# Kernel tuning notes

Measured on AMD Instinct MI355X. Metric: run time of the kernel, lower is better.

Reference implementation:

```python
import jax, jax.numpy as jnp
import numpy as np
from jax import lax

B, CHI, CHO, H, W = 8, 128, 128, 64, 64
K = 3
KK = K * K


def setup_inputs() -> dict:
    key = jax.random.key(0)
    ks = jax.random.split(key, 7)
    x = jax.random.normal(ks[0], (B, CHI, H, W), jnp.float32)
    # small offset-conv weights so sampled offsets stay in a realistic few-pixel range
    off_w = jax.random.normal(ks[1], (3 * KK, CHI, K, K), jnp.float32) * 0.01
    off_b = jnp.zeros((3 * KK,), jnp.float32)
    w = jax.random.normal(ks[2], (CHO, CHI, K, K), jnp.float32) / np.sqrt(CHI * KK).astype(np.float32)
    b = jnp.zeros((CHO,), jnp.float32)
    gamma = jax.random.uniform(ks[3], (CHO,), jnp.float32)  # nn.init.uniform_ on BN weight
    beta = jnp.zeros((CHO,), jnp.float32)
    return {"x": x, "off_w": off_w, "off_b": off_b, "w": w, "b": b, "gamma": gamma, "beta": beta}


def _deform_conv(x, off_w, off_b, w, b):
    """DCNv2 modulated deformable conv, k=3, stride=1, pad=1, dil=1, 1 deform group."""
    B_, C, H_, W_ = x.shape
    # offset/mask branch: plain 3x3 conv -> 27 channels (2*9 offsets, 9 masks)
    om = lax.conv_general_dilated(x, off_w, (1, 1), ((1, 1), (1, 1)),
                                  dimension_numbers=("NCHW", "OIHW", "NCHW"))
    om = om + off_b[None, :, None, None]
    off = om[:, : 2 * KK].reshape(B_, KK, 2, H_, W_)  # [B,9,2,H,W]; ch 2k=y, 2k+1=x
    mask = jax.nn.sigmoid(om[:, 2 * KK:])             # [B,9,H,W]

    ky, kx = jnp.meshgrid(jnp.arange(K, dtype=jnp.float32),
                          jnp.arange(K, dtype=jnp.float32), indexing="ij")
    ky = ky.reshape(KK); kx = kx.reshape(KK)
    # sampling positions: p = p0 - pad + k*dil + offset
    py = off[:, :, 0] + (jnp.arange(H_, dtype=jnp.float32) - 1.0)[None, None, :, None] + ky[None, :, None, None]
    px = off[:, :, 1] + (jnp.arange(W_, dtype=jnp.float32) - 1.0)[None, None, None, :] + kx[None, :, None, None]

    y0 = jnp.floor(py); x0 = jnp.floor(px)
    ly = py - y0; lx = px - x0
    xf = x.reshape(B_, C, H_ * W_)

    def corner(yi, xi, wgt):
        valid = ((yi >= 0) & (yi <= H_ - 1) & (xi >= 0) & (xi <= W_ - 1)).astype(x.dtype)
        yc = jnp.clip(yi, 0, H_ - 1).astype(jnp.int32)
        xc = jnp.clip(xi, 0, W_ - 1).astype(jnp.int32)
        idx = (yc * W_ + xc).reshape(B_, KK * H_ * W_)
        g = jax.vmap(lambda xb, ib: xb[:, ib])(xf, idx).reshape(B_, C, KK, H_, W_)
        return g * (valid * wgt)[:, None]

    val = (corner(y0, x0, (1 - ly) * (1 - lx))
           + corner(y0, x0 + 1, (1 - ly) * lx)
           + corner(y0 + 1, x0, ly * (1 - lx))
           + corner(y0 + 1, x0 + 1, ly * lx))  # [B,C,9,H,W]
    val = val * mask[:, None]  # modulation
    out = jnp.einsum("bckhw,ock->bohw", val, w.reshape(w.shape[0], C, KK))
    return out + b[None, :, None, None]


def reference(x, off_w, off_b, w, b, gamma, beta):
    y = _deform_conv(x, off_w, off_b, w, b)
    # BatchNorm2d in training mode (batch statistics), eps=1e-5, then ReLU
    mean = y.mean(axis=(0, 2, 3))
    var = y.var(axis=(0, 2, 3))
    yn = (y - mean[None, :, None, None]) * lax.rsqrt(var[None, :, None, None] + 1e-5)
    return jax.nn.relu(yn * gamma[None, :, None, None] + beta[None, :, None, None])
```

## Files before the change

kernel.cpp:

```cpp
#include <hip/hip_runtime.h>
#include <hip/hip_bf16.h>
#include <math.h>

#define HH 64
#define WW 64
#define HW 4096
#define LDV 136

typedef __bf16 bf16x8 __attribute__((ext_vector_type(8)));
typedef float floatx4 __attribute__((ext_vector_type(4)));
typedef unsigned int uint4a __attribute__((ext_vector_type(4)));
typedef unsigned int uint2a __attribute__((ext_vector_type(2)));

#define WS_Y    0u
#define WS_XTB  16777216u
#define WS_WTB  25165824u
#define WS_OWB  25460736u
#define WS_PSQ  25534464u

static __device__ inline ushort f2bf(float f) {
  __hip_bfloat16 h = __float2bfloat16(f);
  return __builtin_bit_cast(ushort, h);
}
static __device__ inline float lo16(unsigned int u) { return __builtin_bit_cast(float, u << 16); }
static __device__ inline float hi16(unsigned int u) { return __builtin_bit_cast(float, u & 0xffff0000u); }

static __device__ inline void barrier_lds() {
  asm volatile("s_waitcnt lgkmcnt(0)" ::: "memory");
  __builtin_amdgcn_s_barrier();
}

__global__ __launch_bounds__(256) void k_prep(const float* __restrict__ x,
                                              const float* __restrict__ w,
                                              const float* __restrict__ ow,
                                              ushort* __restrict__ xtb,
                                              ushort* __restrict__ wtb,
                                              ushort* __restrict__ owb,
                                              float* __restrict__ psq) {
  __shared__ float tile[32][33];
  int bid = blockIdx.x;
  if (bid < 4096) {
    int hw0 = (bid & 127) * 32;
    int c0 = ((bid >> 7) & 3) * 32;
    int b = bid >> 9;
    int col = threadIdx.x & 31, row = threadIdx.x >> 5;
    const float* xb = x + ((size_t)b * 128 + c0) * HW + hw0;
#pragma unroll
    for (int i = 0; i < 32; i += 8)
      tile[row + i][col] = xb[(size_t)(row + i) * HW + col];
    __syncthreads();
    int hw = threadIdx.x >> 3, cq = threadIdx.x & 7;
    ushort* xo = xtb + ((size_t)b * HW + hw0) * 128 + c0;
    unsigned int lo = (unsigned int)f2bf(tile[cq * 4 + 0][hw]) |
                      ((unsigned int)f2bf(tile[cq * 4 + 1][hw]) << 16);
    unsigned int hi = (unsigned int)f2bf(tile[cq * 4 + 2][hw]) |
                      ((unsigned int)f2bf(tile[cq * 4 + 3][hw]) << 16);
    uint2a v2 = (uint2a){lo, hi};
    *(uint2a*)(&xo[(size_t)hw * 128 + cq * 4]) = v2;
  } else if (bid < 4096 + 576) {
    int idx = (bid - 4096) * 256 + threadIdx.x;
    int c = idx & 127, o = (idx >> 7) & 127, k = idx >> 14;
    wtb[idx] = f2bf(w[(o * 128 + c) * 9 + k]);
  } else if (bid < 4096 + 720) {
    int j = (bid - 4672) * 256 + threadIdx.x;
    int c = j & 127, o = (j >> 7) & 31, k = j >> 12;
    float v = (o < 27) ? ow[(o * 128 + c) * 9 + k] : 0.f;
    owb[j] = f2bf(v);
  } else {
    for (int i = threadIdx.x; i < 2048; i += 256) psq[i] = 0.f;
  }
}

__global__ __launch_bounds__(256) void k_main(
    const ushort* __restrict__ xtb, const ushort* __restrict__ wtb,
    const ushort* __restrict__ owb, const float* __restrict__ off_b,
    const float* __restrict__ bias, float* __restrict__ y,
    float* __restrict__ psq) {
  __shared__ ushort Vl[2][16 * LDV];
  __shared__ float omL[27 * 16];
  int t = threadIdx.x;
  int lane = t & 63, wv = t >> 6;
  int li = lane & 15, quad = lane >> 4;
  int bx = blockIdx.x;
  int row = bx >> 2, p0b = (bx & 3) * 16;
  int b = blockIdx.y;
  const ushort* xb = xtb + (size_t)b * HW * 128;
  int ch = t & 15;
  int pq = t >> 4;

  int mi = wv;
  floatx4 oacc = (floatx4){0.f, 0.f, 0.f, 0.f};
  uint4a u0;
  auto p1load = [&](int k, uint4a& u) {
    int ky = k / 3, kx = k % 3;
    int ry = row - 1 + ky, cx = p0b + pq - 1 + kx;
    bool v = (ry >= 0 && ry < HH && cx >= 0 && cx < WW);
    int idx = v ? (ry * WW + cx) : 0;
    uint4a a = *(const uint4a*)(xb + (size_t)idx * 128 + ch * 8);
    u = v ? a : (uint4a){0u, 0u, 0u, 0u};
  };
  p1load(0, u0);
  for (int k = 0; k < 9; ++k) {
    *(uint4a*)(&Vl[k & 1][pq * LDV + ch * 8]) = u0;
    if (k < 8) p1load(k + 1, u0);
    barrier_lds();
    if (wv < 2) {
#pragma unroll
      for (int ks = 0; ks < 4; ++ks) {
        bf16x8 bfrag = __builtin_bit_cast(bf16x8,
            *(const uint4a*)(&Vl[k & 1][li * LDV + ks * 32 + quad * 8]));
        bf16x8 afrag = __builtin_bit_cast(bf16x8,
            *(const uint4a*)(&owb[(size_t)(k * 32 + mi * 16 + li) * 128 + ks * 32 + quad * 8]));
        oacc = __builtin_amdgcn_mfma_f32_16x16x32_bf16(afrag, bfrag, oacc, 0, 0, 0);
      }
    }
  }
  if (wv < 2) {
#pragma unroll
    for (int r = 0; r < 4; ++r) {
      int o = mi * 16 + quad * 4 + r;
      if (o < 27) omL[o * 16 + li] = oacc[r] + off_b[o];
    }
  }
  __syncthreads();

  floatx4 macc[2];
#pragma unroll
  for (int i = 0; i < 2; ++i) macc[i] = (floatx4){0.f, 0.f, 0.f, 0.f};

  float wq[4];
  int idx4[4];
  uint4a u[4];

  auto prep = [&](int k) {
    int ky = k / 3, kx = k % 3;
    float offy = omL[(2 * k) * 16 + pq];
    float offx = omL[(2 * k + 1) * 16 + pq];
    float mraw = omL[(18 + k) * 16 + pq];
    float m = 1.f / (1.f + __expf(-mraw));
    float py = offy + (float)(row - 1 + ky);
    float px = offx + (float)(p0b + pq - 1 + kx);
    float y0f = floorf(py), x0f = floorf(px);
    float ly = py - y0f, lx = px - x0f;
    int iy0 = (int)y0f, ix0 = (int)x0f;
    int iy1 = iy0 + 1, ix1 = ix0 + 1;
    float w00 = (1.f - ly) * (1.f - lx) * m, w01 = (1.f - ly) * lx * m;
    float w10 = ly * (1.f - lx) * m, w11 = ly * lx * m;
    if (iy0 < 0 || iy0 > HH - 1) { w00 = 0.f; w01 = 0.f; }
    if (iy1 < 0 || iy1 > HH - 1) { w10 = 0.f; w11 = 0.f; }
    if (ix0 < 0 || ix0 > WW - 1) { w00 = 0.f; w10 = 0.f; }
    if (ix1 < 0 || ix1 > WW - 1) { w01 = 0.f; w11 = 0.f; }
    int cy0 = min(max(iy0, 0), HH - 1), cy1 = min(max(iy1, 0), HH - 1);
    int cx0 = min(max(ix0, 0), WW - 1), cx1 = min(max(ix1, 0), WW - 1);
    idx4[0] = cy0 * WW + cx0;
    idx4[1] = cy0 * WW + cx1;
    idx4[2] = cy1 * WW + cx0;
    idx4[3] = cy1 * WW + cx1;
    wq[0] = w00; wq[1] = w01; wq[2] = w10; wq[3] = w11;
  };
  auto issue = [&]() {
#pragma unroll
    for (int c = 0; c < 4; ++c)
      u[c] = *(const uint4a*)(xb + (size_t)idx4[c] * 128 + ch * 8);
  };

  prep(0);
  issue();
  for (int k = 0; k < 9; ++k) {
    {
      uint4a outv;
#pragma unroll
      for (int e = 0; e < 4; ++e) {
        float rlo = wq[0] * lo16(u[0][e]) + wq[1] * lo16(u[1][e]) +
                    wq[2] * lo16(u[2][e]) + wq[3] * lo16(u[3][e]);
        float rhi = wq[0] * hi16(u[0][e]) + wq[1] * hi16(u[1][e]) +
                    wq[2] * hi16(u[2][e]) + wq[3] * hi16(u[3][e]);
        outv[e] = (unsigned int)f2bf(rlo) | ((unsigned int)f2bf(rhi) << 16);
      }
      *(uint4a*)(&Vl[k & 1][pq * LDV + ch * 8]) = outv;
    }
    if (k < 8) {
      prep(k + 1);
      issue();
    }
    barrier_lds();
    const ushort* Arow = &wtb[(size_t)(k * 128 + wv * 32) * 128];
#pragma unroll
    for (int ks = 0; ks < 4; ++ks) {
      bf16x8 b0 = __builtin_bit_cast(bf16x8,
          *(const uint4a*)(&Vl[k & 1][li * LDV + ks * 32 + quad * 8]));
      bf16x8 a0 = __builtin_bit_cast(bf16x8,
          *(const uint4a*)(Arow + (size_t)(li)*128 + ks * 32 + quad * 8));
      bf16x8 a1 = __builtin_bit_cast(bf16x8,
          *(const uint4a*)(Arow + (size_t)(16 + li) * 128 + ks * 32 + quad * 8));
      macc[0] = __builtin_amdgcn_mfma_f32_16x16x32_bf16(a0, b0, macc[0], 0, 0, 0);
      macc[1] = __builtin_amdgcn_mfma_f32_16x16x32_bf16(a1, b0, macc[1], 0, 0, 0);
    }
  }

  int slot = bx & 7;
#pragma unroll
  for (int ot = 0; ot < 2; ++ot)
#pragma unroll
    for (int r = 0; r < 4; ++r) {
      int o = wv * 32 + ot * 16 + quad * 4 + r;
      float v = macc[ot][r] + bias[o];
      y[((size_t)(b * 128 + o)) * HW + row * 64 + p0b + li] = v;
      float s = v, q = v * v;
#pragma unroll
      for (int m = 1; m < 16; m <<= 1) {
        s += __shfl_xor(s, m, 64);
        q += __shfl_xor(q, m, 64);
      }
      if (li == 0) {
        atomicAdd(&psq[slot * 256 + o], s);
        atomicAdd(&psq[slot * 256 + 128 + o], q);
      }
    }
}

__global__ __launch_bounds__(256) void k_norm(const float* __restrict__ y,
                                              const float* __restrict__ psq,
                                              const float* __restrict__ gamma,
                                              const float* __restrict__ beta,
                                              float* __restrict__ out) {
  int blk = blockIdx.x;
  int o = (blk >> 2) & 127;
  float s = 0.f, q = 0.f;
#pragma unroll
  for (int j = 0; j < 8; ++j) {
    s += psq[j * 256 + o];
    q += psq[j * 256 + 128 + o];
  }
  float mean = s * (1.f / 32768.f);
  float var = q * (1.f / 32768.f) - mean * mean;
  float scale = gamma[o] * rsqrtf(var + 1e-5f);
  float shift = beta[o] - mean * scale;
  int i4 = blk * 256 + threadIdx.x;
  float4 v = ((const float4*)y)[i4];
  float4 r;
  r.x = fmaxf(v.x * scale + shift, 0.f);
  r.y = fmaxf(v.y * scale + shift, 0.f);
  r.z = fmaxf(v.z * scale + shift, 0.f);
  r.w = fmaxf(v.w * scale + shift, 0.f);
  ((float4*)out)[i4] = r;
}

extern "C" void kernel_launch(void* const* d_in, const int* in_sizes, int n_in,
                              void* d_out, int out_size, void* d_ws, size_t ws_size,
                              hipStream_t stream) {
  const float* x     = (const float*)d_in[0];
  const float* off_w = (const float*)d_in[1];
  const float* off_b = (const float*)d_in[2];
  const float* w     = (const float*)d_in[3];
  const float* bias  = (const float*)d_in[4];
  const float* gamma = (const float*)d_in[5];
  const float* beta  = (const float*)d_in[6];
  float* out = (float*)d_out;
  char* ws = (char*)d_ws;

  float* y    = (float*)(ws + WS_Y);
  ushort* xtb = (ushort*)(ws + WS_XTB);
  ushort* wtb = (ushort*)(ws + WS_WTB);
  ushort* owb = (ushort*)(ws + WS_OWB);
  float* psq  = (float*)(ws + WS_PSQ);

  k_prep<<<4817, 256, 0, stream>>>(x, w, off_w, xtb, wtb, owb, psq);
  k_main<<<dim3(256, 8), 256, 0, stream>>>(xtb, wtb, owb, off_b, bias, y, psq);
  k_norm<<<4096, 256, 0, stream>>>(y, psq, gamma, beta, out);
}
```

Before: 185.3 us.

## Double pixel tile per block to reuse weight fragments across two MFMA columns

Each k_main block now handles 32 pixels instead of 16, halving the grid. Every wave loads its weight A-fragments once and applies them to two pixel sub-tiles, cutting global weight traffic per output. The offset-conv phase now uses all four waves instead of two. The unrolled loops keep two sets of gather registers in flight, prefetching two taps ahead. The cost is higher register pressure, fewer blocks (1024) to spread over the CUs, and more LDS per block.

```diff
diff --git a/kernel.cpp b/kernel.cpp
--- a/kernel.cpp
+++ b/kernel.cpp
@@ -76,70 +76,84 @@
     const ushort* __restrict__ owb, const float* __restrict__ off_b,
     const float* __restrict__ bias, float* __restrict__ y,
     float* __restrict__ psq) {
-  __shared__ ushort Vl[2][16 * LDV];
-  __shared__ float omL[27 * 16];
+  __shared__ ushort Vl[2][32 * LDV];
+  __shared__ float omL[27 * 32];
   int t = threadIdx.x;
   int lane = t & 63, wv = t >> 6;
   int li = lane & 15, quad = lane >> 4;
-  int bx = blockIdx.x;
-  int row = bx >> 2, p0b = (bx & 3) * 16;
+  int hr = blockIdx.x;
+  int row = hr >> 1, p0b = (hr & 1) * 32;
   int b = blockIdx.y;
   const ushort* xb = xtb + (size_t)b * HW * 128;
   int ch = t & 15;
   int pq = t >> 4;
 
-  int mi = wv;
+  int mi = wv & 1, ni = wv >> 1;
   floatx4 oacc = (floatx4){0.f, 0.f, 0.f, 0.f};
-  uint4a u0;
-  auto p1load = [&](int k, uint4a& u) {
+  uint4a uA0, uB0, uA1, uB1;
+  auto p1load = [&](int k, int p, uint4a& u) {
     int ky = k / 3, kx = k % 3;
-    int ry = row - 1 + ky, cx = p0b + pq - 1 + kx;
+    int ry = row - 1 + ky, cx = p0b + p - 1 + kx;
     bool v = (ry >= 0 && ry < HH && cx >= 0 && cx < WW);
     int idx = v ? (ry * WW + cx) : 0;
     uint4a a = *(const uint4a*)(xb + (size_t)idx * 128 + ch * 8);
     u = v ? a : (uint4a){0u, 0u, 0u, 0u};
   };
-  p1load(0, u0);
-  for (int k = 0; k < 9; ++k) {
-    *(uint4a*)(&Vl[k & 1][pq * LDV + ch * 8]) = u0;
-    if (k < 8) p1load(k + 1, u0);
-    barrier_lds();
-    if (wv < 2) {
-#pragma unroll
-      for (int ks = 0; ks < 4; ++ks) {
-        bf16x8 bfrag = __builtin_bit_cast(bf16x8,
-            *(const uint4a*)(&Vl[k & 1][li * LDV + ks * 32 + quad * 8]));
-        bf16x8 afrag = __builtin_bit_cast(bf16x8,
-            *(const uint4a*)(&owb[(size_t)(k * 32 + mi * 16 + li) * 128 + ks * 32 + quad * 8]));
-        oacc = __builtin_amdgcn_mfma_f32_16x16x32_bf16(afrag, bfrag, oacc, 0, 0, 0);
-      }
-    }
-  }
-  if (wv < 2) {
-#pragma unroll
-    for (int r = 0; r < 4; ++r) {
-      int o = mi * 16 + quad * 4 + r;
-      if (o < 27) omL[o * 16 + li] = oacc[r] + off_b[o];
-    }
+
+#define PH1_STEP(K, UA, UB, BUF, KP)                                          \
+  do {                                                                        \
+    *(uint4a*)(&Vl[BUF][pq * LDV + ch * 8]) = UA;                             \
+    *(uint4a*)(&Vl[BUF][(pq + 16) * LDV + ch * 8]) = UB;                      \
+    if ((KP) < 9) { p1load((KP), pq, UA); p1load((KP), pq + 16, UB); }        \
+    barrier_lds();                                                            \
+    _Pragma("unroll")                                                         \
+    for (int ks = 0; ks < 4; ++ks) {                                          \
+      bf16x8 bfrag = __builtin_bit_cast(bf16x8,                               \
+          *(const uint4a*)(&Vl[BUF][(ni * 16 + li) * LDV + ks * 32 + quad * 8])); \
+      bf16x8 afrag = __builtin_bit_cast(bf16x8,                               \
+          *(const uint4a*)(&owb[(size_t)((K) * 32 + mi * 16 + li) * 128 + ks * 32 + quad * 8])); \
+      oacc = __builtin_amdgcn_mfma_f32_16x16x32_bf16(afrag, bfrag, oacc, 0, 0, 0); \
+    }                                                                         \
+  } while (0)
+
+  p1load(0, pq, uA0); p1load(0, pq + 16, uB0);
+  p1load(1, pq, uA1); p1load(1, pq + 16, uB1);
+  PH1_STEP(0, uA0, uB0, 0, 2);
+  PH1_STEP(1, uA1, uB1, 1, 3);
+  PH1_STEP(2, uA0, uB0, 0, 4);
+  PH1_STEP(3, uA1, uB1, 1, 5);
+  PH1_STEP(4, uA0, uB0, 0, 6);
+  PH1_STEP(5, uA1, uB1, 1, 7);
+  PH1_STEP(6, uA0, uB0, 0, 8);
+  PH1_STEP(7, uA1, uB1, 1, 9);
+  PH1_STEP(8, uA0, uB0, 0, 9);
+#undef PH1_STEP
+
+#pragma unroll
+  for (int r = 0; r < 4; ++r) {
+    int o = mi * 16 + quad * 4 + r;
+    if (o < 27) omL[o * 32 + ni * 16 + li] = oacc[r] + off_b[o];
   }
   __syncthreads();
 
-  floatx4 macc[2];
-#pragma unroll
-  for (int i = 0; i < 2; ++i) macc[i] = (floatx4){0.f, 0.f, 0.f, 0.f};
-
-  float wq[4];
-  int idx4[4];
-  uint4a u[4];
-
-  auto prep = [&](int k) {
+  floatx4 macc[2][2];
+#pragma unroll
+  for (int i = 0; i < 2; ++i)
+#pragma unroll
+    for (int j = 0; j < 2; ++j) macc[i][j] = (floatx4){0.f, 0.f, 0.f, 0.f};
+
+  float wqA0[4], wqB0[4], wqA1[4], wqB1[4];
+  int idxA[4], idxB[4];
+  uint4a U0[8], U1[8];
+
+  auto prep = [&](int k, int p, float* wq, int* idx4) {
     int ky = k / 3, kx = k % 3;
-    float offy = omL[(2 * k) * 16 + pq];
-    float offx = omL[(2 * k + 1) * 16 + pq];
-    float mraw = omL[(18 + k) * 16 + pq];
+    float offy = omL[(2 * k) * 32 + p];
+    float offx = omL[(2 * k + 1) * 32 + p];
+    float mraw = omL[(18 + k) * 32 + p];
     float m = 1.f / (1.f + __expf(-mraw));
     float py = offy + (float)(row - 1 + ky);
-    float px = offx + (float)(p0b + pq - 1 + kx);
+    float px = offx + (float)(p0b + p - 1 + kx);
     float y0f = floorf(py), x0f = floorf(px);
     float ly = py - y0f, lx = px - x0f;
     int iy0 = (int)y0f, ix0 = (int)x0f;
@@ -158,55 +172,82 @@
     idx4[3] = cy1 * WW + cx1;
     wq[0] = w00; wq[1] = w01; wq[2] = w10; wq[3] = w11;
   };
-  auto issue = [&]() {
+  auto issueTo = [&](uint4a* U) {
 #pragma unroll
     for (int c = 0; c < 4; ++c)
-      u[c] = *(const uint4a*)(xb + (size_t)idx4[c] * 128 + ch * 8);
+      U[c] = *(const uint4a*)(xb + (size_t)idxA[c] * 128 + ch * 8);
+#pragma unroll
+    for (int c = 0; c < 4; ++c)
+      U[4 + c] = *(const uint4a*)(xb + (size_t)idxB[c] * 128 + ch * 8);
   };
 
-  prep(0);
-  issue();
-  for (int k = 0; k < 9; ++k) {
-    {
-      uint4a outv;
-#pragma unroll
-      for (int e = 0; e < 4; ++e) {
-        float rlo = wq[0] * lo16(u[0][e]) + wq[1] * lo16(u[1][e]) +
-                    wq[2] * lo16(u[2][e]) + wq[3] * lo16(u[3][e]);
-        float rhi = wq[0] * hi16(u[0][e]) + wq[1] * hi16(u[1][e]) +
-                    wq[2] * hi16(u[2][e]) + wq[3] * hi16(u[3][e]);
-        outv[e] = (unsigned int)f2bf(rlo) | ((unsigned int)f2bf(rhi) << 16);
-      }
-      *(uint4a*)(&Vl[k & 1][pq * LDV + ch * 8]) = outv;
-    }
-    if (k < 8) {
-      prep(k + 1);
-      issue();
-    }
-    barrier_lds();
-    const ushort* Arow = &wtb[(size_t)(k * 128 + wv * 32) * 128];
-#pragma unroll
-    for (int ks = 0; ks < 4; ++ks) {
-      bf16x8 b0 = __builtin_bit_cast(bf16x8,
-          *(const uint4a*)(&Vl[k & 1][li * LDV + ks * 32 + quad * 8]));
-      bf16x8 a0 = __builtin_bit_cast(bf16x8,
-          *(const uint4a*)(Arow + (size_t)(li)*128 + ks * 32 + quad * 8));
-      bf16x8 a1 = __builtin_bit_cast(bf16x8,
-          *(const uint4a*)(Arow + (size_t)(16 + li) * 128 + ks * 32 + quad * 8));
-      macc[0] = __builtin_amdgcn_mfma_f32_16x16x32_bf16(a0, b0, macc[0], 0, 0, 0);
-      macc[1] = __builtin_amdgcn_mfma_f32_16x16x32_bf16(a1, b0, macc[1], 0, 0, 0);
-    }
-  }
-
-  int slot = bx & 7;
+#define CONVW(U, WQ, ROWP, BUF)                                               \
+  do {                                                                        \
+    uint4a outv;                                                              \
+    _Pragma("unroll")                                                         \
+    for (int e = 0; e < 4; ++e) {                                             \
+      float rlo = WQ[0] * lo16(U[0][e]) + WQ[1] * lo16(U[1][e]) +             \
+                  WQ[2] * lo16(U[2][e]) + WQ[3] * lo16(U[3][e]);              \
+      float rhi = WQ[0] * hi16(U[0][e]) + WQ[1] * hi16(U[1][e]) +             \
+                  WQ[2] * hi16(U[2][e]) + WQ[3] * hi16(U[3][e]);              \
+      outv[e] = (unsigned int)f2bf(rlo) | ((unsigned int)f2bf(rhi) << 16);    \
+    }                                                                         \
+    *(uint4a*)(&Vl[BUF][(ROWP)*LDV + ch * 8]) = outv;                         \
+  } while (0)
+
+#define PH2_STEP(K, U, WQA, WQB, BUF, KP)                                     \
+  do {                                                                        \
+    CONVW(U, WQA, pq, BUF);                                                   \
+    CONVW((U + 4), WQB, (pq + 16), BUF);                                      \
+    if ((KP) < 9) {                                                           \
+      prep((KP), pq, WQA, idxA);                                              \
+      prep((KP), pq + 16, WQB, idxB);                                         \
+      issueTo(U);                                                             \
+    }                                                                         \
+    barrier_lds();                                                            \
+    const ushort* Arow = &wtb[(size_t)((K) * 128 + wv * 32) * 128];           \
+    _Pragma("unroll")                                                         \
+    for (int ks = 0; ks < 4; ++ks) {                                          \
+      bf16x8 b0 = __builtin_bit_cast(bf16x8,                                  \
+          *(const uint4a*)(&Vl[BUF][(li)*LDV + ks * 32 + quad * 8]));         \
+      bf16x8 b1 = __builtin_bit_cast(bf16x8,                                  \
+          *(const uint4a*)(&Vl[BUF][(16 + li) * LDV + ks * 32 + quad * 8]));  \
+      bf16x8 a0 = __builtin_bit_cast(bf16x8,                                  \
+          *(const uint4a*)(Arow + (size_t)(li)*128 + ks * 32 + quad * 8));    \
+      bf16x8 a1 = __builtin_bit_cast(bf16x8,                                  \
+          *(const uint4a*)(Arow + (size_t)(16 + li) * 128 + ks * 32 + quad * 8)); \
+      macc[0][0] = __builtin_amdgcn_mfma_f32_16x16x32_bf16(a0, b0, macc[0][0], 0, 0, 0); \
+      macc[0][1] = __builtin_amdgcn_mfma_f32_16x16x32_bf16(a0, b1, macc[0][1], 0, 0, 0); \
+      macc[1][0] = __builtin_amdgcn_mfma_f32_16x16x32_bf16(a1, b0, macc[1][0], 0, 0, 0); \
+      macc[1][1] = __builtin_amdgcn_mfma_f32_16x16x32_bf16(a1, b1, macc[1][1], 0, 0, 0); \
+    }                                                                         \
+  } while (0)
+
+  prep(0, pq, wqA0, idxA); prep(0, pq + 16, wqB0, idxB); issueTo(U0);
+  prep(1, pq, wqA1, idxA); prep(1, pq + 16, wqB1, idxB); issueTo(U1);
+  PH2_STEP(0, U0, wqA0, wqB0, 0, 2);
+  PH2_STEP(1, U1, wqA1, wqB1, 1, 3);
+  PH2_STEP(2, U0, wqA0, wqB0, 0, 4);
+  PH2_STEP(3, U1, wqA1, wqB1, 1, 5);
+  PH2_STEP(4, U0, wqA0, wqB0, 0, 6);
+  PH2_STEP(5, U1, wqA1, wqB1, 1, 7);
+  PH2_STEP(6, U0, wqA0, wqB0, 0, 8);
+  PH2_STEP(7, U1, wqA1, wqB1, 1, 9);
+  PH2_STEP(8, U0, wqA0, wqB0, 0, 9);
+#undef PH2_STEP
+#undef CONVW
+
+  int slot = hr & 7;
 #pragma unroll
   for (int ot = 0; ot < 2; ++ot)
 #pragma unroll
     for (int r = 0; r < 4; ++r) {
       int o = wv * 32 + ot * 16 + quad * 4 + r;
-      float v = macc[ot][r] + bias[o];
-      y[((size_t)(b * 128 + o)) * HW + row * 64 + p0b + li] = v;
-      float s = v, q = v * v;
+      float v0 = macc[ot][0][r] + bias[o];
+      float v1 = macc[ot][1][r] + bias[o];
+      y[((size_t)(b * 128 + o)) * HW + row * 64 + p0b + li] = v0;
+      y[((size_t)(b * 128 + o)) * HW + row * 64 + p0b + 16 + li] = v1;
+      float s = v0 + v1, q = v0 * v0 + v1 * v1;
 #pragma unroll
       for (int m = 1; m < 16; m <<= 1) {
         s += __shfl_xor(s, m, 64);
@@ -266,6 +307,6 @@
   float* psq  = (float*)(ws + WS_PSQ);
 
   k_prep<<<4817, 256, 0, stream>>>(x, w, off_w, xtb, wtb, owb, psq);
-  k_main<<<dim3(256, 8), 256, 0, stream>>>(xtb, wtb, owb, off_b, bias, y, psq);
+  k_main<<<dim3(128, 8), 256, 0, stream>>>(xtb, wtb, owb, off_b, bias, y, psq);
   k_norm<<<4096, 256, 0, stream>>>(y, psq, gamma, beta, out);
 }
```

Result: faster. 174.3 us (-5.9%).

## Double k_main pixel tile to 32 with 512-thread blocks and batch-interleaved grid

Applied to the files above, without the earlier changes.

Each k_main block now covers 32 pixels with 8 waves, and each wave handles 16 output channels across two pixel sub-tiles, so every weight fragment feeds two MFMAs. The offset-conv phase uses four waves to cover the larger tile, and the grid is flattened with the batch index in the low bits so neighbouring blocks work on different images. The stats slot count doubles to 16 to spread atomics, and k_norm's block indexing is remapped to follow the new order. The intent is to cut global weight-fragment loads per FLOP and improve occupancy, at the cost of more LDS per block, larger barrier groups and the launch_bounds(512, 8) register limit.

```diff
diff --git a/kernel.cpp b/kernel.cpp
--- a/kernel.cpp
+++ b/kernel.cpp
@@ -6,6 +6,7 @@
 #define WW 64
 #define HW 4096
 #define LDV 136
+#define NSLOT 16
 
 typedef __bf16 bf16x8 __attribute__((ext_vector_type(8)));
 typedef float floatx4 __attribute__((ext_vector_type(4)));
@@ -67,28 +68,29 @@
     float v = (o < 27) ? ow[(o * 128 + c) * 9 + k] : 0.f;
     owb[j] = f2bf(v);
   } else {
-    for (int i = threadIdx.x; i < 2048; i += 256) psq[i] = 0.f;
-  }
-}
-
-__global__ __launch_bounds__(256) void k_main(
+    for (int i = threadIdx.x; i < NSLOT * 256; i += 256) psq[i] = 0.f;
+  }
+}
+
+__global__ __launch_bounds__(512, 8) void k_main(
     const ushort* __restrict__ xtb, const ushort* __restrict__ wtb,
     const ushort* __restrict__ owb, const float* __restrict__ off_b,
     const float* __restrict__ bias, float* __restrict__ y,
     float* __restrict__ psq) {
-  __shared__ ushort Vl[2][16 * LDV];
-  __shared__ float omL[27 * 16];
+  __shared__ ushort Vl[2][32 * LDV];
+  __shared__ float omL[27 * 32];
   int t = threadIdx.x;
   int lane = t & 63, wv = t >> 6;
-  int li = lane & 15, quad = lane >> 4;
-  int bx = blockIdx.x;
-  int row = bx >> 2, p0b = (bx & 3) * 16;
-  int b = blockIdx.y;
+  int li = lane & 15, quad = (lane >> 4) & 3;
+  int bid = blockIdx.x;
+  int b = bid & 7;
+  int hr = bid >> 3;
+  int row = hr >> 1, p0b = (hr & 1) * 32;
   const ushort* xb = xtb + (size_t)b * HW * 128;
   int ch = t & 15;
   int pq = t >> 4;
 
-  int mi = wv;
+  int mi = wv & 1, ni = (wv >> 1) & 1;
   floatx4 oacc = (floatx4){0.f, 0.f, 0.f, 0.f};
   uint4a u0;
   auto p1load = [&](int k, uint4a& u) {
@@ -104,29 +106,29 @@
     *(uint4a*)(&Vl[k & 1][pq * LDV + ch * 8]) = u0;
     if (k < 8) p1load(k + 1, u0);
     barrier_lds();
-    if (wv < 2) {
+    if (wv < 4) {
 #pragma unroll
       for (int ks = 0; ks < 4; ++ks) {
         bf16x8 bfrag = __builtin_bit_cast(bf16x8,
-            *(const uint4a*)(&Vl[k & 1][li * LDV + ks * 32 + quad * 8]));
+            *(const uint4a*)(&Vl[k & 1][(ni * 16 + li) * LDV + ks * 32 + quad * 8]));
         bf16x8 afrag = __builtin_bit_cast(bf16x8,
             *(const uint4a*)(&owb[(size_t)(k * 32 + mi * 16 + li) * 128 + ks * 32 + quad * 8]));
         oacc = __builtin_amdgcn_mfma_f32_16x16x32_bf16(afrag, bfrag, oacc, 0, 0, 0);
       }
     }
   }
-  if (wv < 2) {
+  if (wv < 4) {
 #pragma unroll
     for (int r = 0; r < 4; ++r) {
       int o = mi * 16 + quad * 4 + r;
-      if (o < 27) omL[o * 16 + li] = oacc[r] + off_b[o];
+      if (o < 27) omL[o * 32 + ni * 16 + li] = oacc[r] + off_b[o];
     }
   }
   __syncthreads();
 
   floatx4 macc[2];
-#pragma unroll
-  for (int i = 0; i < 2; ++i) macc[i] = (floatx4){0.f, 0.f, 0.f, 0.f};
+  macc[0] = (floatx4){0.f, 0.f, 0.f, 0.f};
+  macc[1] = (floatx4){0.f, 0.f, 0.f, 0.f};
 
   float wq[4];
   int idx4[4];
@@ -134,9 +136,9 @@
 
   auto prep = [&](int k) {
     int ky = k / 3, kx = k % 3;
-    float offy = omL[(2 * k) * 16 + pq];
-    float offx = omL[(2 * k + 1) * 16 + pq];
-    float mraw = omL[(18 + k) * 16 + pq];
+    float offy = omL[(2 * k) * 32 + pq];
+    float offx = omL[(2 * k + 1) * 32 + pq];
+    float mraw = omL[(18 + k) * 32 + pq];
     float m = 1.f / (1.f + __expf(-mraw));
     float py = offy + (float)(row - 1 + ky);
     float px = offx + (float)(p0b + pq - 1 + kx);
@@ -184,39 +186,39 @@
       issue();
     }
     barrier_lds();
-    const ushort* Arow = &wtb[(size_t)(k * 128 + wv * 32) * 128];
+    const ushort* Arow = &wtb[(size_t)(k * 128 + wv * 16) * 128];
 #pragma unroll
     for (int ks = 0; ks < 4; ++ks) {
       bf16x8 b0 = __builtin_bit_cast(bf16x8,
-          *(const uint4a*)(&Vl[k & 1][li * LDV + ks * 32 + quad * 8]));
+          *(const uint4a*)(&Vl[k & 1][(li)*LDV + ks * 32 + quad * 8]));
+      bf16x8 b1 = __builtin_bit_cast(bf16x8,
+          *(const uint4a*)(&Vl[k & 1][(16 + li) * LDV + ks * 32 + quad * 8]));
       bf16x8 a0 = __builtin_bit_cast(bf16x8,
           *(const uint4a*)(Arow + (size_t)(li)*128 + ks * 32 + quad * 8));
-      bf16x8 a1 = __builtin_bit_cast(bf16x8,
-          *(const uint4a*)(Arow + (size_t)(16 + li) * 128 + ks * 32 + quad * 8));
       macc[0] = __builtin_amdgcn_mfma_f32_16x16x32_bf16(a0, b0, macc[0], 0, 0, 0);
-      macc[1] = __builtin_amdgcn_mfma_f32_16x16x32_bf16(a1, b0, macc[1], 0, 0, 0);
-    }
-  }
-
-  int slot = bx & 7;
-#pragma unroll
-  for (int ot = 0; ot < 2; ++ot)
-#pragma unroll
-    for (int r = 0; r < 4; ++r) {
-      int o = wv * 32 + ot * 16 + quad * 4 + r;
-      float v = macc[ot][r] + bias[o];
-      y[((size_t)(b * 128 + o)) * HW + row * 64 + p0b + li] = v;
-      float s = v, q = v * v;
-#pragma unroll
-      for (int m = 1; m < 16; m <<= 1) {
-        s += __shfl_xor(s, m, 64);
-        q += __shfl_xor(q, m, 64);
-      }
-      if (li == 0) {
-        atomicAdd(&psq[slot * 256 + o], s);
-        atomicAdd(&psq[slot * 256 + 128 + o], q);
-      }
-    }
+      macc[1] = __builtin_amdgcn_mfma_f32_16x16x32_bf16(a0, b1, macc[1], 0, 0, 0);
+    }
+  }
+
+  int slot = bid & (NSLOT - 1);
+#pragma unroll
+  for (int r = 0; r < 4; ++r) {
+    int o = wv * 16 + quad * 4 + r;
+    float v0 = macc[0][r] + bias[o];
+    float v1 = macc[1][r] + bias[o];
+    y[((size_t)(b * 128 + o)) * HW + row * 64 + p0b + li] = v0;
+    y[((size_t)(b * 128 + o)) * HW + row * 64 + p0b + 16 + li] = v1;
+    float s = v0 + v1, q = v0 * v0 + v1 * v1;
+#pragma unroll
+    for (int m = 1; m < 16; m <<= 1) {
+      s += __shfl_xor(s, m, 64);
+      q += __shfl_xor(q, m, 64);
+    }
+    if (li == 0) {
+      atomicAdd(&psq[slot * 256 + o], s);
+      atomicAdd(&psq[slot * 256 + 128 + o], q);
+    }
+  }
 }
 
 __global__ __launch_bounds__(256) void k_norm(const float* __restrict__ y,
@@ -225,10 +227,12 @@
                                               const float* __restrict__ beta,
                                               float* __restrict__ out) {
   int blk = blockIdx.x;
-  int o = (blk >> 2) & 127;
+  int b = blk & 7;
+  int o = (blk >> 3) & 127;
+  int qseg = blk >> 10;
   float s = 0.f, q = 0.f;
 #pragma unroll
-  for (int j = 0; j < 8; ++j) {
+  for (int j = 0; j < NSLOT; ++j) {
     s += psq[j * 256 + o];
     q += psq[j * 256 + 128 + o];
   }
@@ -236,7 +240,7 @@
   float var = q * (1.f / 32768.f) - mean * mean;
   float scale = gamma[o] * rsqrtf(var + 1e-5f);
   float shift = beta[o] - mean * scale;
-  int i4 = blk * 256 + threadIdx.x;
+  int i4 = (b * 128 + o) * 1024 + qseg * 256 + threadIdx.x;
   float4 v = ((const float4*)y)[i4];
   float4 r;
   r.x = fmaxf(v.x * scale + shift, 0.f);
@@ -266,6 +270,6 @@
   float* psq  = (float*)(ws + WS_PSQ);
 
   k_prep<<<4817, 256, 0, stream>>>(x, w, off_w, xtb, wtb, owb, psq);
-  k_main<<<dim3(256, 8), 256, 0, stream>>>(xtb, wtb, owb, off_b, bias, y, psq);
+  k_main<<<1024, 512, 0, stream>>>(xtb, wtb, owb, off_b, bias, y, psq);
   k_norm<<<4096, 256, 0, stream>>>(y, psq, gamma, beta, out);
 }
```

Result: faster. 156.1 us (-15.7%).
